# Kernel optimization log

Hardware: AMD Instinct MI355X
Metric: run time of the kernel (lower is better)

Reference implementation:

```python
import jax, jax.numpy as jnp
import numpy as np

N, D, IN_F, OUT_F = 1024, 32, 128, 128


def setup_inputs() -> dict:
    key = jax.random.key(0)
    k1, k2, k3, k4, k5 = jax.random.split(key, 5)
    bound = 1.0 / np.sqrt(IN_F)
    return {
        "u": jax.random.normal(k1, (N, IN_F), dtype=jnp.float32),
        "dudx": jax.random.normal(k2, (N, D, IN_F), dtype=jnp.float32),
        "d2ud2x": jax.random.normal(k3, (N, D, D, IN_F), dtype=jnp.float32),
        "K": jax.random.uniform(k4, (IN_F, OUT_F), dtype=jnp.float32, minval=-bound, maxval=bound),
        "b": jax.random.uniform(k5, (OUT_F,), dtype=jnp.float32, minval=-bound, maxval=bound),
    }


def reference(u, dudx, d2ud2x, K, b):
    # f(u(x)) = tanh(u @ K + b), with forward-mode gradient & Hessian propagation.
    z = u @ K + b                      # (N, out)
    f = jnp.tanh(z)
    dsig = 1.0 - f * f                 # tanh'(z)
    d2sig = -2.0 * f * dsig            # tanh''(z)

    # dfdx[n,d,o] = sum_i dudx[n,d,i] * dsig[n,o] * K[i,o]
    A = jnp.einsum('ndi,io->ndo', dudx, K)        # dudx @ K, (N, d, out)
    dfdx = dsig[:, None, :] * A                   # (N, d, out)

    # Same math as the torch code's (N,in,in,out) outer-product tensor contracted
    # against dudx, exploiting d2fd2x_local[n,i,j,o] = d2sig[n,o]*K[i,o]*K[j,o].
    h1 = d2sig[:, None, None, :] * A[:, :, None, :] * A[:, None, :, :]   # (N, d, d, out)
    B = jnp.einsum('ndei,io->ndeo', d2ud2x, K)                           # (N, d, d, out)
    d2fd2x = h1 + dsig[:, None, None, :] * B

    return f, dfdx, d2fd2x
```

## Files before the change

### kernel.cpp

```cpp
#include <hip/hip_runtime.h>


typedef __bf16 bf16x8 __attribute__((ext_vector_type(8)));
typedef float f32x4 __attribute__((ext_vector_type(4)));

__device__ __forceinline__ unsigned int pk2bf(float a, float b) {
    unsigned int ua = __builtin_bit_cast(unsigned int, a);
    unsigned int ub = __builtin_bit_cast(unsigned int, b);
    ua = (ua + 0x7FFFu + ((ua >> 16) & 1u)) >> 16;
    ub = (ub + 0x7FFFu + ((ub >> 16) & 1u)) >> 16;
    return ua | (ub << 16);
}

__global__ __launch_bounds__(256) void k_prep(const float* __restrict__ u,
                                              const float* __restrict__ K,
                                              const float* __restrict__ b,
                                              float* __restrict__ f_out,
                                              float* __restrict__ dsig,
                                              float* __restrict__ d2sig) {
    __shared__ float us[16][128];
    const int t = threadIdx.x;
    const int blk = blockIdx.x;
    {
        int row = t >> 4, c = (t & 15) * 8;
        const float4* src = reinterpret_cast<const float4*>(u + (blk * 16 + row) * 128 + c);
        float4 v0 = src[0], v1 = src[1];
        *reinterpret_cast<float4*>(&us[row][c])     = v0;
        *reinterpret_cast<float4*>(&us[row][c + 4]) = v1;
    }
    __syncthreads();
    const int o = t & 127;
    const int rr = (t >> 7) * 8;
    float acc[8] = {0.f, 0.f, 0.f, 0.f, 0.f, 0.f, 0.f, 0.f};
    for (int i = 0; i < 128; ++i) {
        float kv = K[i * 128 + o];
#pragma unroll
        for (int j = 0; j < 8; ++j) acc[j] = fmaf(us[rr + j][i], kv, acc[j]);
    }
    const float bv = b[o];
#pragma unroll
    for (int j = 0; j < 8; ++j) {
        int row = blk * 16 + rr + j;
        float z = acc[j] + bv;
        float fv = tanhf(z);
        float ds = 1.0f - fv * fv;
        f_out[row * 128 + o] = fv;
        dsig[row * 128 + o] = ds;
        d2sig[row * 128 + o] = -2.0f * fv * ds;
    }
}

__global__ __launch_bounds__(128) void k_kt(const float* __restrict__ K,
                                            unsigned short* __restrict__ kt) {
    const int o = blockIdx.x, i = threadIdx.x;
    unsigned int v = __builtin_bit_cast(unsigned int, K[i * 128 + o]);
    v = (v + 0x7FFFu + ((v >> 16) & 1u)) >> 16;
    kt[o * 128 + i] = (unsigned short)v;
}

#define LPAD 136

__device__ __forceinline__ void stage_kt(const unsigned short* __restrict__ kt,
                                         unsigned short* Ks, int t) {
#pragma unroll
    for (int p = 0; p < 8; ++p) {
        int row = p * 16 + (t >> 4);
        int k0 = (t & 15) * 8;
        uint4 v = *reinterpret_cast<const uint4*>(kt + row * 128 + k0);
        *reinterpret_cast<uint4*>(&Ks[row * LPAD + k0]) = v;
    }
}

__device__ __forceinline__ void stage_x(const float* __restrict__ X, int R0,
                                        unsigned short* Xs, int t) {
#pragma unroll
    for (int p = 0; p < 4; ++p) {
        int row = p * 16 + (t >> 4);
        int c0 = (t & 15) * 8;
        const float4* s = reinterpret_cast<const float4*>(X + (size_t)(R0 + row) * 128 + c0);
        float4 v0 = s[0], v1 = s[1];
        uint4 w;
        w.x = pk2bf(v0.x, v0.y);
        w.y = pk2bf(v0.z, v0.w);
        w.z = pk2bf(v1.x, v1.y);
        w.w = pk2bf(v1.z, v1.w);
        *reinterpret_cast<uint4*>(&Xs[row * LPAD + c0]) = w;
    }
}

__device__ __forceinline__ void gemm_tile(const unsigned short* Xs,
                                          const unsigned short* Ks,
                                          int m0l, int q, int l, f32x4 acc[8]) {
#pragma unroll
    for (int s = 0; s < 4; ++s) {
        bf16x8 a = *reinterpret_cast<const bf16x8*>(&Xs[(m0l + l) * LPAD + s * 32 + q * 8]);
#pragma unroll
        for (int c = 0; c < 8; ++c) {
            bf16x8 bf = *reinterpret_cast<const bf16x8*>(&Ks[(c * 16 + l) * LPAD + s * 32 + q * 8]);
            acc[c] = __builtin_amdgcn_mfma_f32_16x16x32_bf16(a, bf, acc[c], 0, 0, 0);
        }
    }
}

__global__ __launch_bounds__(256) void k_dfdx(const float* __restrict__ dudx,
                                              const unsigned short* __restrict__ kt,
                                              const float* __restrict__ dsig,
                                              float* __restrict__ wsA,
                                              float* __restrict__ dfdx_out) {
    __shared__ unsigned short Ks[128 * LPAD];
    __shared__ unsigned short Xs[64 * LPAD];
    const int t = threadIdx.x;
    const int R0 = blockIdx.x * 64;

    stage_kt(kt, Ks, t);
    stage_x(dudx, R0, Xs, t);
    __syncthreads();

    const int w = t >> 6, lane = t & 63, q = lane >> 4, l = lane & 15;
    f32x4 acc[8];
#pragma unroll
    for (int c = 0; c < 8; ++c) acc[c] = (f32x4){0.f, 0.f, 0.f, 0.f};
    gemm_tile(Xs, Ks, w * 16, q, l, acc);

    const int m0 = R0 + w * 16;
    const int n = m0 >> 5;
    const float* dsp = dsig + n * 128;
    float* ap = wsA + (size_t)m0 * 128;
    float* dp = dfdx_out + (size_t)m0 * 128;
#pragma unroll
    for (int c = 0; c < 8; ++c) {
        int o = c * 16 + l;
        float ds = dsp[o];
#pragma unroll
        for (int r = 0; r < 4; ++r) {
            int ri = q * 4 + r;
            float a = acc[c][r];
            ap[ri * 128 + o] = a;
            dp[ri * 128 + o] = ds * a;
        }
    }
}

__global__ __launch_bounds__(256) void k_hess(const float* __restrict__ X,
                                              const unsigned short* __restrict__ kt,
                                              const float* __restrict__ dsig,
                                              const float* __restrict__ d2sig,
                                              const float* __restrict__ wsA,
                                              float* __restrict__ out_h,
                                              int nchunks) {
    __shared__ unsigned short Ks[128 * LPAD];
    __shared__ unsigned short Xs[64 * LPAD];
    const int t = threadIdx.x;
    stage_kt(kt, Ks, t);

    const int w = t >> 6, lane = t & 63, q = lane >> 4, l = lane & 15;

    for (int chunk = blockIdx.x; chunk < nchunks; chunk += gridDim.x) {
        __syncthreads();
        const int R0 = chunk * 64;
        stage_x(X, R0, Xs, t);
        __syncthreads();

        f32x4 acc[8];
#pragma unroll
        for (int c = 0; c < 8; ++c) acc[c] = (f32x4){0.f, 0.f, 0.f, 0.f};
        gemm_tile(Xs, Ks, w * 16, q, l, acc);

        const int m0 = R0 + w * 16;
        const int n = m0 >> 10;
        const int d = (m0 >> 5) & 31;
        const int e0 = m0 & 31;
        const float* dsp = dsig + n * 128;
        const float* d2p = d2sig + n * 128;
        const float* Adp = wsA + (size_t)(n * 32 + d) * 128;
        const float* Aep = wsA + (size_t)(n * 32 + e0) * 128;
        float* outp = out_h + (size_t)m0 * 128;
#pragma unroll
        for (int c = 0; c < 8; ++c) {
            int o = c * 16 + l;
            float ds = dsp[o];
            float tt = d2p[o] * Adp[o];
#pragma unroll
            for (int r = 0; r < 4; ++r) {
                int ri = q * 4 + r;
                float Ae = Aep[(size_t)ri * 128 + o];
                outp[(size_t)ri * 128 + o] = fmaf(ds, acc[c][r], tt * Ae);
            }
        }
    }
}

extern "C" void kernel_launch(void* const* d_in, const int* in_sizes, int n_in,
                              void* d_out, int out_size, void* d_ws, size_t ws_size,
                              hipStream_t stream) {
    const float* u      = (const float*)d_in[0];
    const float* dudx   = (const float*)d_in[1];
    const float* d2ud2x = (const float*)d_in[2];
    const float* K      = (const float*)d_in[3];
    const float* b      = (const float*)d_in[4];

    float* out = (float*)d_out;
    float* f_out    = out;
    float* dfdx_out = out + 131072;
    float* hess_out = out + 131072 + 4194304;

    float* ws = (float*)d_ws;
    float* dsig  = ws;
    float* d2sig = ws + 131072;
    unsigned short* kt = (unsigned short*)(ws + 262144);
    float* wsA   = ws + 262144 + 8192;

    k_prep<<<64, 256, 0, stream>>>(u, K, b, f_out, dsig, d2sig);
    k_kt<<<128, 128, 0, stream>>>(K, kt);
    k_dfdx<<<512, 256, 0, stream>>>(dudx, kt, dsig, wsA, dfdx_out);
    k_hess<<<2048, 256, 0, stream>>>(d2ud2x, kt, dsig, d2sig, wsA, hess_out, 16384);
}
```

Baseline: 903.9 us.

## Keep K fragments in registers and feed MFMA directly from global loads

Removes LDS staging in the dfdx and Hessian GEMM kernels. Each wave now loads its K^T bf16 fragments into registers once, then reads its own 16-row tile of X straight from global memory, converts it to bf16 and issues the MFMAs. This drops the block-level __syncthreads and LDS traffic, and the grid-stride loop moves from 64-row block chunks to per-wave 16-row tiles. The cost is about 128 VGPRs per lane held for K fragments, with launch_bounds(256,2) capping occupancy, and global loads of X that are less coalesced than the old staged loads.

```diff
diff --git a/kernel.cpp b/kernel.cpp
--- a/kernel.cpp
+++ b/kernel.cpp
@@ -58,71 +58,54 @@
     kt[o * 128 + i] = (unsigned short)v;
 }
 
-#define LPAD 136
+__device__ __forceinline__ void load_kfrag(const unsigned short* __restrict__ kt,
+                                           int q, int l, bf16x8 (&kf)[8][4]) {
+#pragma unroll
+    for (int c = 0; c < 8; ++c)
+#pragma unroll
+        for (int s = 0; s < 4; ++s)
+            kf[c][s] = *reinterpret_cast<const bf16x8*>(kt + (c * 16 + l) * 128 + s * 32 + q * 8);
+}
 
-__device__ __forceinline__ void stage_kt(const unsigned short* __restrict__ kt,
-                                         unsigned short* Ks, int t) {
+__device__ __forceinline__ void tile_gemm(const float* __restrict__ xrow, int q,
+                                          const bf16x8 (&kf)[8][4], f32x4 (&acc)[8]) {
+    float4 v0[4], v1[4];
 #pragma unroll
-    for (int p = 0; p < 8; ++p) {
-        int row = p * 16 + (t >> 4);
-        int k0 = (t & 15) * 8;
-        uint4 v = *reinterpret_cast<const uint4*>(kt + row * 128 + k0);
-        *reinterpret_cast<uint4*>(&Ks[row * LPAD + k0]) = v;
+    for (int s = 0; s < 4; ++s) {
+        const float4* p = reinterpret_cast<const float4*>(xrow) + (s * 8 + q * 2);
+        v0[s] = p[0];
+        v1[s] = p[1];
+    }
+#pragma unroll
+    for (int s = 0; s < 4; ++s) {
+        uint4 wv;
+        wv.x = pk2bf(v0[s].x, v0[s].y);
+        wv.y = pk2bf(v0[s].z, v0[s].w);
+        wv.z = pk2bf(v1[s].x, v1[s].y);
+        wv.w = pk2bf(v1[s].z, v1[s].w);
+        bf16x8 a = __builtin_bit_cast(bf16x8, wv);
+#pragma unroll
+        for (int c = 0; c < 8; ++c)
+            acc[c] = __builtin_amdgcn_mfma_f32_16x16x32_bf16(a, kf[c][s], acc[c], 0, 0, 0);
     }
 }
 
-__device__ __forceinline__ void stage_x(const float* __restrict__ X, int R0,
-                                        unsigned short* Xs, int t) {
-#pragma unroll
-    for (int p = 0; p < 4; ++p) {
-        int row = p * 16 + (t >> 4);
-        int c0 = (t & 15) * 8;
-        const float4* s = reinterpret_cast<const float4*>(X + (size_t)(R0 + row) * 128 + c0);
-        float4 v0 = s[0], v1 = s[1];
-        uint4 w;
-        w.x = pk2bf(v0.x, v0.y);
-        w.y = pk2bf(v0.z, v0.w);
-        w.z = pk2bf(v1.x, v1.y);
-        w.w = pk2bf(v1.z, v1.w);
-        *reinterpret_cast<uint4*>(&Xs[row * LPAD + c0]) = w;
-    }
-}
+__global__ __launch_bounds__(256, 2) void k_dfdx(const float* __restrict__ dudx,
+                                                 const unsigned short* __restrict__ kt,
+                                                 const float* __restrict__ dsig,
+                                                 float* __restrict__ wsA,
+                                                 float* __restrict__ dfdx_out) {
+    const int t = threadIdx.x, w = t >> 6, lane = t & 63, q = lane >> 4, l = lane & 15;
+    bf16x8 kf[8][4];
+    load_kfrag(kt, q, l, kf);
 
-__device__ __forceinline__ void gemm_tile(const unsigned short* Xs,
-                                          const unsigned short* Ks,
-                                          int m0l, int q, int l, f32x4 acc[8]) {
-#pragma unroll
-    for (int s = 0; s < 4; ++s) {
-        bf16x8 a = *reinterpret_cast<const bf16x8*>(&Xs[(m0l + l) * LPAD + s * 32 + q * 8]);
-#pragma unroll
-        for (int c = 0; c < 8; ++c) {
-            bf16x8 bf = *reinterpret_cast<const bf16x8*>(&Ks[(c * 16 + l) * LPAD + s * 32 + q * 8]);
-            acc[c] = __builtin_amdgcn_mfma_f32_16x16x32_bf16(a, bf, acc[c], 0, 0, 0);
-        }
-    }
-}
-
-__global__ __launch_bounds__(256) void k_dfdx(const float* __restrict__ dudx,
-                                              const unsigned short* __restrict__ kt,
-                                              const float* __restrict__ dsig,
-                                              float* __restrict__ wsA,
-                                              float* __restrict__ dfdx_out) {
-    __shared__ unsigned short Ks[128 * LPAD];
-    __shared__ unsigned short Xs[64 * LPAD];
-    const int t = threadIdx.x;
-    const int R0 = blockIdx.x * 64;
-
-    stage_kt(kt, Ks, t);
-    stage_x(dudx, R0, Xs, t);
-    __syncthreads();
-
-    const int w = t >> 6, lane = t & 63, q = lane >> 4, l = lane & 15;
+    const int wid = blockIdx.x * 4 + w;
+    const int m0 = wid * 16;
     f32x4 acc[8];
 #pragma unroll
     for (int c = 0; c < 8; ++c) acc[c] = (f32x4){0.f, 0.f, 0.f, 0.f};
-    gemm_tile(Xs, Ks, w * 16, q, l, acc);
+    tile_gemm(dudx + (size_t)(m0 + l) * 128, q, kf, acc);
 
-    const int m0 = R0 + w * 16;
     const int n = m0 >> 5;
     const float* dsp = dsig + n * 128;
     float* ap = wsA + (size_t)m0 * 128;
@@ -141,32 +124,26 @@
     }
 }
 
-__global__ __launch_bounds__(256) void k_hess(const float* __restrict__ X,
-                                              const unsigned short* __restrict__ kt,
-                                              const float* __restrict__ dsig,
-                                              const float* __restrict__ d2sig,
-                                              const float* __restrict__ wsA,
-                                              float* __restrict__ out_h,
-                                              int nchunks) {
-    __shared__ unsigned short Ks[128 * LPAD];
-    __shared__ unsigned short Xs[64 * LPAD];
-    const int t = threadIdx.x;
-    stage_kt(kt, Ks, t);
+__global__ __launch_bounds__(256, 2) void k_hess(const float* __restrict__ X,
+                                                 const unsigned short* __restrict__ kt,
+                                                 const float* __restrict__ dsig,
+                                                 const float* __restrict__ d2sig,
+                                                 const float* __restrict__ wsA,
+                                                 float* __restrict__ out_h,
+                                                 int ntiles) {
+    const int t = threadIdx.x, w = t >> 6, lane = t & 63, q = lane >> 4, l = lane & 15;
+    bf16x8 kf[8][4];
+    load_kfrag(kt, q, l, kf);
 
-    const int w = t >> 6, lane = t & 63, q = lane >> 4, l = lane & 15;
-
-    for (int chunk = blockIdx.x; chunk < nchunks; chunk += gridDim.x) {
-        __syncthreads();
-        const int R0 = chunk * 64;
-        stage_x(X, R0, Xs, t);
-        __syncthreads();
-
+    const int wid = blockIdx.x * 4 + w;
+    const int nw = gridDim.x * 4;
+    for (int tile = wid; tile < ntiles; tile += nw) {
+        const int m0 = tile * 16;
         f32x4 acc[8];
 #pragma unroll
         for (int c = 0; c < 8; ++c) acc[c] = (f32x4){0.f, 0.f, 0.f, 0.f};
-        gemm_tile(Xs, Ks, w * 16, q, l, acc);
+        tile_gemm(X + (size_t)(m0 + l) * 128, q, kf, acc);
 
-        const int m0 = R0 + w * 16;
         const int n = m0 >> 10;
         const int d = (m0 >> 5) & 31;
         const int e0 = m0 & 31;
@@ -213,5 +190,5 @@
     k_prep<<<64, 256, 0, stream>>>(u, K, b, f_out, dsig, d2sig);
     k_kt<<<128, 128, 0, stream>>>(K, kt);
     k_dfdx<<<512, 256, 0, stream>>>(dudx, kt, dsig, wsA, dfdx_out);
-    k_hess<<<2048, 256, 0, stream>>>(d2ud2x, kt, dsig, d2sig, wsA, hess_out, 16384);
+    k_hess<<<2048, 256, 0, stream>>>(d2ud2x, kt, dsig, d2sig, wsA, hess_out, 65536);
 }
```

Measured after the change: 930.9 us. +3.0%, slower.
